# Optimization experiments

Measured on AMD Instinct MI355X. Metric: run time of the kernel, lower is better.

Reference implementation:

```python
import jax, jax.numpy as jnp
import numpy as np

B, T, D, DO = 8, 2048, 1024, 1024

def setup_inputs() -> dict:
    key = jax.random.key(0)
    ks = jax.random.split(key, 7)
    s = 1.0 / np.sqrt(D)
    return {
        "input_tensor": jax.random.normal(ks[0], (B, T, D), dtype=jnp.float32),
        "Wq": jax.random.uniform(ks[1], (D, D), jnp.float32, -s, s),
        "bq": jax.random.uniform(ks[2], (D,), jnp.float32, -s, s),
        "Wk": jax.random.uniform(ks[3], (D, D), jnp.float32, -s, s),
        "bk": jax.random.uniform(ks[4], (D,), jnp.float32, -s, s),
        "Wv": jax.random.uniform(ks[5], (D, DO), jnp.float32, -s, s),
        "bv": jax.random.uniform(ks[6], (DO,), jnp.float32, -s, s),
    }

def reference(input_tensor, Wq, bq, Wk, bk, Wv, bv):
    scale = jnp.sqrt(jnp.float32(input_tensor.shape[-1]))
    q = input_tensor @ Wq + bq            # [B,T,D]
    k = input_tensor @ Wk + bk            # [B,T,D]
    v = input_tensor @ Wv + bv            # [B,T,DO]
    scores = jnp.einsum('btd,bsd->bts', q, k) / scale  # [B,T,T]
    attn = jax.nn.softmax(scores, axis=-1)
    return jnp.einsum('bts,bso->bto', attn, v)         # [B,T,DO]
```

## Files before the change

kernel.cpp:

```cpp
#include <hip/hip_runtime.h>
#include <stdint.h>

typedef unsigned short u16;
typedef __attribute__((ext_vector_type(4))) float    floatx4;
typedef __attribute__((ext_vector_type(8))) __bf16   bf16x8;
typedef __attribute__((ext_vector_type(2))) unsigned int uintx2;
typedef __attribute__((ext_vector_type(4))) unsigned int uintx4;

__device__ inline u16 f2bf(float f) {
  unsigned int u = __builtin_bit_cast(unsigned int, f);
  u += 0x7fffu + ((u >> 16) & 1u);
  return (u16)(u >> 16);
}

#define GLD16(gsrc, ldst)                                                        \
  __builtin_amdgcn_global_load_lds(                                              \
      (__attribute__((address_space(1))) void*)(gsrc),                           \
      (__attribute__((address_space(3))) void*)(ldst), 16, 0, 0)

__global__ __launch_bounds__(256) void prep_kernel(const float* __restrict__ x,
                                                   const float* __restrict__ Wq,
                                                   const float* __restrict__ Wk,
                                                   const float* __restrict__ Wv,
                                                   u16* __restrict__ xb,
                                                   u16* __restrict__ WT) {
  const int z = blockIdx.z;
  const int tid = threadIdx.y * 32 + threadIdx.x;
  if (z >= 3) {
    long blk = (long)(z - 3) * 1024 + blockIdx.y * 32 + blockIdx.x;
    long i = (blk * 256 + tid) * 8;
    floatx4 a = *(const floatx4*)(x + i);
    floatx4 b = *(const floatx4*)(x + i + 4);
    uintx4 o;
    o[0] = (unsigned)f2bf(a[0]) | ((unsigned)f2bf(a[1]) << 16);
    o[1] = (unsigned)f2bf(a[2]) | ((unsigned)f2bf(a[3]) << 16);
    o[2] = (unsigned)f2bf(b[0]) | ((unsigned)f2bf(b[1]) << 16);
    o[3] = (unsigned)f2bf(b[2]) | ((unsigned)f2bf(b[3]) << 16);
    *(uintx4*)(xb + i) = o;
    return;
  }
  __shared__ float tile[32][33];
  const float* W = (z == 0) ? Wq : (z == 1) ? Wk : Wv;
  u16* dst = WT + (long)z * 1024 * 1024;
  int bx = blockIdx.x * 32, by = blockIdx.y * 32;
  int tx = threadIdx.x, ty = threadIdx.y;
  for (int i = 0; i < 32; i += 8)
    tile[ty + i][tx] = W[(long)(by + ty + i) * 1024 + bx + tx];
  __syncthreads();
  for (int i = 0; i < 32; i += 8)
    dst[(long)(bx + ty + i) * 1024 + by + tx] = f2bf(tile[tx][ty + i]);
}

#define BM 256
#define BN 256
#define BK 64

template <int MODE, int GN>
__global__ __launch_bounds__(512, 2)
void gemm_bt(const u16* __restrict__ Aall, const u16* __restrict__ Ball,
             void* __restrict__ Call, void* __restrict__ C2,
             const float* __restrict__ bias, const float* __restrict__ bias2,
             float* __restrict__ lsum,
             int M, int N, int K, long aStride, long bStride, long cStride) {
  __shared__ __align__(16) u16 As[2][BM * BK];
  __shared__ __align__(16) u16 Bs[2][BN * BK];

  const int z = blockIdx.z;
  const u16* A  = Aall + (long)z * aStride;
  const u16* Bt = Ball + (long)z * bStride;

  int m_idx, n_idx;
  if (GN > 0) {
    const int tiles_n = gridDim.x, tiles_m = gridDim.y;
    int bid = blockIdx.y * tiles_n + blockIdx.x;
    int per_group = GN * tiles_m;
    int g = bid / per_group;
    int rem = bid - g * per_group;
    n_idx = g * GN + rem % GN;
    m_idx = rem / GN;
  } else {
    m_idx = blockIdx.y; n_idx = blockIdx.x;
  }

  const int tid  = threadIdx.x;
  const int m0   = m_idx * BM;
  const int n0   = n_idx * BN;
  const int wave = tid >> 6;
  const int lane = tid & 63;
  const int wm   = (wave >> 2) * 128;
  const int wn   = (wave & 3) * 64;
  const int l15  = lane & 15;
  const int quad = lane >> 4;

  floatx4 acc[8][4];
  floatx4 zero = {0.f, 0.f, 0.f, 0.f};
#pragma unroll
  for (int i = 0; i < 8; ++i)
#pragma unroll
    for (int j = 0; j < 4; ++j) acc[i][j] = zero;

  int rows[4], cols[4];
#pragma unroll
  for (int i = 0; i < 4; ++i) {
    int ci = i * 512 + tid;
    int r = ci >> 3, sc = ci & 7;
    rows[i] = r; cols[i] = (sc ^ (r & 7)) * 8;
  }

  auto stage = [&](int kt, u16* as, u16* bs) {
#pragma unroll
    for (int i = 0; i < 4; ++i)
      GLD16(A + (long)(m0 + rows[i]) * K + kt + cols[i], as + (i * 512 + tid) * 8);
#pragma unroll
    for (int i = 0; i < 4; ++i)
      GLD16(Bt + (long)(n0 + rows[i]) * K + kt + cols[i], bs + (i * 512 + tid) * 8);
  };

  const int nt = K / BK;
  stage(0, As[0], Bs[0]);
  stage(BK, As[1], Bs[1]);

  for (int t = 0; t < nt; ++t) {
    const int cur = t & 1;
    const u16* Ab = As[cur];
    const u16* Bb = Bs[cur];
    if (t + 1 < nt) asm volatile("s_waitcnt vmcnt(8)" ::: "memory");
    else            asm volatile("s_waitcnt vmcnt(0)" ::: "memory");
    __builtin_amdgcn_s_barrier();
    __builtin_amdgcn_sched_barrier(0);

    bf16x8 af0[8], bf0[4], af1[8], bf1[4];
#pragma unroll
    for (int mi = 0; mi < 8; ++mi) {
      int r = wm + mi * 16 + l15;
      af0[mi] = *(const bf16x8*)(Ab + (r * 8 + (quad ^ (r & 7))) * 8);
    }
#pragma unroll
    for (int ni = 0; ni < 4; ++ni) {
      int r = wn + ni * 16 + l15;
      bf0[ni] = *(const bf16x8*)(Bb + (r * 8 + (quad ^ (r & 7))) * 8);
    }
    __builtin_amdgcn_s_setprio(1);
#pragma unroll
    for (int mi = 0; mi < 8; ++mi)
#pragma unroll
      for (int ni = 0; ni < 4; ++ni)
        acc[mi][ni] = __builtin_amdgcn_mfma_f32_16x16x32_bf16(
            bf0[ni], af0[mi], acc[mi][ni], 0, 0, 0);
    __builtin_amdgcn_s_setprio(0);
#pragma unroll
    for (int mi = 0; mi < 8; ++mi) {
      int r = wm + mi * 16 + l15;
      af1[mi] = *(const bf16x8*)(Ab + (r * 8 + ((4 + quad) ^ (r & 7))) * 8);
    }
#pragma unroll
    for (int ni = 0; ni < 4; ++ni) {
      int r = wn + ni * 16 + l15;
      bf1[ni] = *(const bf16x8*)(Bb + (r * 8 + ((4 + quad) ^ (r & 7))) * 8);
    }
    asm volatile("s_waitcnt lgkmcnt(0)" ::: "memory");
    __builtin_amdgcn_sched_barrier(0);
    __builtin_amdgcn_s_barrier();
    __builtin_amdgcn_sched_barrier(0);
    if (t + 2 < nt) stage((t + 2) * BK, As[cur], Bs[cur]);
    __builtin_amdgcn_s_setprio(1);
#pragma unroll
    for (int mi = 0; mi < 8; ++mi)
#pragma unroll
      for (int ni = 0; ni < 4; ++ni)
        acc[mi][ni] = __builtin_amdgcn_mfma_f32_16x16x32_bf16(
            bf1[ni], af1[mi], acc[mi][ni], 0, 0, 0);
    __builtin_amdgcn_s_setprio(0);
  }

#pragma unroll
  for (int mi = 0; mi < 8; ++mi) {
    const int row = m0 + wm + mi * 16 + l15;
    if (MODE == 2) {
      u16* C = (u16*)Call + (long)z * cStride;
      float rs = 0.f;
#pragma unroll
      for (int ni = 0; ni < 4; ++ni) {
        int colb = n0 + wn + ni * 16 + quad * 4;
        floatx4 v = acc[mi][ni];
        float e0 = __expf(v[0] * 0.03125f), e1 = __expf(v[1] * 0.03125f);
        float e2 = __expf(v[2] * 0.03125f), e3 = __expf(v[3] * 0.03125f);
        rs += (e0 + e1) + (e2 + e3);
        uintx2 o;
        o[0] = (unsigned)f2bf(e0) | ((unsigned)f2bf(e1) << 16);
        o[1] = (unsigned)f2bf(e2) | ((unsigned)f2bf(e3) << 16);
        *(uintx2*)(C + (long)row * N + colb) = o;
      }
      rs += __shfl_xor(rs, 16);
      rs += __shfl_xor(rs, 32);
      if (quad == 0) atomicAdd(lsum + (long)z * 2048 + row, rs);
    } else if (MODE == 3) {
      float* C = (float*)Call + (long)z * cStride;
      float inv = 1.0f / lsum[(long)z * 2048 + row];
#pragma unroll
      for (int ni = 0; ni < 4; ++ni) {
        int colb = n0 + wn + ni * 16 + quad * 4;
        floatx4 v = acc[mi][ni];
        floatx4 o = {v[0] * inv, v[1] * inv, v[2] * inv, v[3] * inv};
        *(floatx4*)(C + (long)row * N + colb) = o;
      }
    } else if (MODE == 0) {
#pragma unroll
      for (int ni = 0; ni < 4; ++ni) {
        int colb = n0 + wn + ni * 16 + quad * 4;
        u16* C = (colb < 1024) ? (u16*)Call : (u16*)C2;
        const float* bp = (colb < 1024) ? bias + colb : bias2 + (colb - 1024);
        floatx4 b = *(const floatx4*)bp;
        floatx4 v = acc[mi][ni];
        uintx2 o;
        o[0] = (unsigned)f2bf(v[0] + b[0]) | ((unsigned)f2bf(v[1] + b[1]) << 16);
        o[1] = (unsigned)f2bf(v[2] + b[2]) | ((unsigned)f2bf(v[3] + b[3]) << 16);
        *(uintx2*)(C + (long)row * 1024 + (colb & 1023)) = o;
      }
    } else {
      u16* C = (u16*)Call;
      float b = bias[row];
#pragma unroll
      for (int ni = 0; ni < 4; ++ni) {
        int colb = n0 + wn + ni * 16 + quad * 4;
        long base = ((long)(colb >> 11) * 1024) * 2048 + (colb & 2047);
        floatx4 v = acc[mi][ni];
        uintx2 o;
        o[0] = (unsigned)f2bf(v[0] + b) | ((unsigned)f2bf(v[1] + b) << 16);
        o[1] = (unsigned)f2bf(v[2] + b) | ((unsigned)f2bf(v[3] + b) << 16);
        *(uintx2*)(C + base + (long)row * 2048) = o;
      }
    }
  }
}

extern "C" void kernel_launch(void* const* d_in, const int* in_sizes, int n_in,
                              void* d_out, int out_size, void* d_ws, size_t ws_size,
                              hipStream_t stream) {
  const float* x  = (const float*)d_in[0];
  const float* Wq = (const float*)d_in[1];
  const float* bq = (const float*)d_in[2];
  const float* Wk = (const float*)d_in[3];
  const float* bk = (const float*)d_in[4];
  const float* Wv = (const float*)d_in[5];
  const float* bv = (const float*)d_in[6];
  float* out = (float*)d_out;

  const long BT = 16384;
  u16* xb = (u16*)d_ws;
  u16* WT = xb + BT * 1024;
  u16* qb = WT + 3L * 1024 * 1024;
  u16* kb = qb + BT * 1024;
  u16* vT = kb + BT * 1024;
  u16* S  = vT + BT * 1024;
  float* lsum = (float*)(S + 8L * 2048 * 2048);

  hipMemsetAsync(lsum, 0, 8 * 2048 * sizeof(float), stream);

  prep_kernel<<<dim3(32, 32, 11), dim3(32, 8), 0, stream>>>(x, Wq, Wk, Wv, xb, WT);

  gemm_bt<0, 8><<<dim3(8, 64, 1), 512, 0, stream>>>(
      xb, WT, qb, kb, bq, bk, nullptr, 16384, 2048, 1024, 0, 0, 0);
  gemm_bt<1, 8><<<dim3(64, 4, 1), 512, 0, stream>>>(
      WT + 2L * 1024 * 1024, xb, vT, nullptr, bv, nullptr, nullptr,
      1024, 16384, 1024, 0, 0, 0);
  gemm_bt<2, 8><<<dim3(8, 8, 8), 512, 0, stream>>>(
      qb, kb, S, nullptr, nullptr, nullptr, lsum,
      2048, 2048, 1024, 2048L * 1024, 2048L * 1024, 2048L * 2048);
  gemm_bt<3, 4><<<dim3(4, 8, 8), 512, 0, stream>>>(
      S, vT, out, nullptr, nullptr, nullptr, lsum,
      2048, 1024, 2048, 2048L * 2048, 1024L * 2048, 2048L * 1024);
}
```

Baseline: 384.4 us.

## Interleave global-to-LDS staging with four MFMA sub-phases per K tile

Restructures the GEMM main loop from two half-K MFMA phases with one bulk prefetch into four quarter phases. Each phase issues a slice of the next tile's A/B global_load_lds copies, with finer-grained vmcnt waits and barriers. The goal is to spread memory traffic across the MFMA work and cut register pressure from fragment arrays, so load latency hides better. In exchange it adds barriers per iteration and a fragile ordering of which buffer slices are overwritten when.

```diff
diff --git a/kernel.cpp b/kernel.cpp
--- a/kernel.cpp
+++ b/kernel.cpp
@@ -107,70 +107,130 @@
     rows[i] = r; cols[i] = (sc ^ (r & 7)) * 8;
   }
 
-  auto stage = [&](int kt, u16* as, u16* bs) {
-#pragma unroll
-    for (int i = 0; i < 4; ++i)
-      GLD16(A + (long)(m0 + rows[i]) * K + kt + cols[i], as + (i * 512 + tid) * 8);
-#pragma unroll
-    for (int i = 0; i < 4; ++i)
-      GLD16(Bt + (long)(n0 + rows[i]) * K + kt + cols[i], bs + (i * 512 + tid) * 8);
+  auto stageA = [&](int kt2, u16* dst, int b) {
+    GLD16(A + (long)(m0 + rows[b]) * K + kt2 + cols[b], dst + (b * 512 + tid) * 8);
   };
+  auto stageB = [&](int kt2, u16* dst, int b) {
+    GLD16(Bt + (long)(n0 + rows[b]) * K + kt2 + cols[b], dst + (b * 512 + tid) * 8);
+  };
 
   const int nt = K / BK;
-  stage(0, As[0], Bs[0]);
-  stage(BK, As[1], Bs[1]);
+
+  stageA(0, As[0], 0); stageA(0, As[0], 2);
+  stageB(0, Bs[0], 0); stageB(0, Bs[0], 1);
+  stageB(0, Bs[0], 2); stageB(0, Bs[0], 3);
+  stageA(0, As[0], 1); stageA(0, As[0], 3);
+  stageA(BK, As[1], 0); stageA(BK, As[1], 2);
+  asm volatile("s_waitcnt vmcnt(2)" ::: "memory");
+  __builtin_amdgcn_sched_barrier(0);
+  __builtin_amdgcn_s_barrier();
+  __builtin_amdgcn_sched_barrier(0);
 
   for (int t = 0; t < nt; ++t) {
     const int cur = t & 1;
     const u16* Ab = As[cur];
     const u16* Bb = Bs[cur];
-    if (t + 1 < nt) asm volatile("s_waitcnt vmcnt(8)" ::: "memory");
-    else            asm volatile("s_waitcnt vmcnt(0)" ::: "memory");
-    __builtin_amdgcn_s_barrier();
-    __builtin_amdgcn_sched_barrier(0);
-
-    bf16x8 af0[8], bf0[4], af1[8], bf1[4];
-#pragma unroll
-    for (int mi = 0; mi < 8; ++mi) {
+    u16* Ac = As[cur];
+    u16* An = As[cur ^ 1];
+    u16* Bn = Bs[cur ^ 1];
+    const int ktn = (t + 1) * BK;
+    const bool st1 = (t + 1 < nt);
+    const bool st2 = (t + 2 < nt);
+    bf16x8 afA[4], afB[4], bfr[4];
+
+#pragma unroll
+    for (int mi = 0; mi < 4; ++mi) {
       int r = wm + mi * 16 + l15;
-      af0[mi] = *(const bf16x8*)(Ab + (r * 8 + (quad ^ (r & 7))) * 8);
+      afA[mi] = *(const bf16x8*)(Ab + (r * 8 + (quad ^ (r & 7))) * 8);
     }
 #pragma unroll
     for (int ni = 0; ni < 4; ++ni) {
       int r = wn + ni * 16 + l15;
-      bf0[ni] = *(const bf16x8*)(Bb + (r * 8 + (quad ^ (r & 7))) * 8);
-    }
+      bfr[ni] = *(const bf16x8*)(Bb + (r * 8 + (quad ^ (r & 7))) * 8);
+    }
+    if (st1) { stageB(ktn, Bn, 0); stageB(ktn, Bn, 1); }
+    if (st1) asm volatile("s_waitcnt vmcnt(4)" ::: "memory");
+    else     asm volatile("s_waitcnt vmcnt(0)" ::: "memory");
+    asm volatile("s_waitcnt lgkmcnt(0)" ::: "memory");
+    __builtin_amdgcn_sched_barrier(0);
+    __builtin_amdgcn_s_barrier();
+    __builtin_amdgcn_sched_barrier(0);
     __builtin_amdgcn_s_setprio(1);
 #pragma unroll
-    for (int mi = 0; mi < 8; ++mi)
+    for (int mi = 0; mi < 4; ++mi)
 #pragma unroll
       for (int ni = 0; ni < 4; ++ni)
         acc[mi][ni] = __builtin_amdgcn_mfma_f32_16x16x32_bf16(
-            bf0[ni], af0[mi], acc[mi][ni], 0, 0, 0);
+            bfr[ni], afA[mi], acc[mi][ni], 0, 0, 0);
     __builtin_amdgcn_s_setprio(0);
-#pragma unroll
-    for (int mi = 0; mi < 8; ++mi) {
+    __builtin_amdgcn_sched_barrier(0);
+
+#pragma unroll
+    for (int mi = 0; mi < 4; ++mi) {
+      int r = wm + (4 + mi) * 16 + l15;
+      afB[mi] = *(const bf16x8*)(Ab + (r * 8 + (quad ^ (r & 7))) * 8);
+    }
+    if (st1) { stageB(ktn, Bn, 2); stageB(ktn, Bn, 3); }
+    asm volatile("s_waitcnt lgkmcnt(0)" ::: "memory");
+    __builtin_amdgcn_sched_barrier(0);
+    __builtin_amdgcn_s_barrier();
+    __builtin_amdgcn_sched_barrier(0);
+    __builtin_amdgcn_s_setprio(1);
+#pragma unroll
+    for (int mi = 0; mi < 4; ++mi)
+#pragma unroll
+      for (int ni = 0; ni < 4; ++ni)
+        acc[4 + mi][ni] = __builtin_amdgcn_mfma_f32_16x16x32_bf16(
+            bfr[ni], afB[mi], acc[4 + mi][ni], 0, 0, 0);
+    __builtin_amdgcn_s_setprio(0);
+    __builtin_amdgcn_sched_barrier(0);
+
+#pragma unroll
+    for (int mi = 0; mi < 4; ++mi) {
       int r = wm + mi * 16 + l15;
-      af1[mi] = *(const bf16x8*)(Ab + (r * 8 + ((4 + quad) ^ (r & 7))) * 8);
+      afA[mi] = *(const bf16x8*)(Ab + (r * 8 + ((4 + quad) ^ (r & 7))) * 8);
     }
 #pragma unroll
     for (int ni = 0; ni < 4; ++ni) {
       int r = wn + ni * 16 + l15;
-      bf1[ni] = *(const bf16x8*)(Bb + (r * 8 + ((4 + quad) ^ (r & 7))) * 8);
-    }
+      bfr[ni] = *(const bf16x8*)(Bb + (r * 8 + ((4 + quad) ^ (r & 7))) * 8);
+    }
+    if (st1) { stageA(ktn, An, 1); stageA(ktn, An, 3); }
     asm volatile("s_waitcnt lgkmcnt(0)" ::: "memory");
     __builtin_amdgcn_sched_barrier(0);
     __builtin_amdgcn_s_barrier();
     __builtin_amdgcn_sched_barrier(0);
-    if (t + 2 < nt) stage((t + 2) * BK, As[cur], Bs[cur]);
     __builtin_amdgcn_s_setprio(1);
 #pragma unroll
-    for (int mi = 0; mi < 8; ++mi)
+    for (int mi = 0; mi < 4; ++mi)
 #pragma unroll
       for (int ni = 0; ni < 4; ++ni)
         acc[mi][ni] = __builtin_amdgcn_mfma_f32_16x16x32_bf16(
-            bf1[ni], af1[mi], acc[mi][ni], 0, 0, 0);
+            bfr[ni], afA[mi], acc[mi][ni], 0, 0, 0);
     __builtin_amdgcn_s_setprio(0);
+    __builtin_amdgcn_sched_barrier(0);
+
+#pragma unroll
+    for (int mi = 0; mi < 4; ++mi) {
+      int r = wm + (4 + mi) * 16 + l15;
+      afB[mi] = *(const bf16x8*)(Ab + (r * 8 + ((4 + quad) ^ (r & 7))) * 8);
+    }
+    if (st2) { stageA(ktn + BK, Ac, 0); stageA(ktn + BK, Ac, 2); }
+    if (st2)      asm volatile("s_waitcnt vmcnt(4)" ::: "memory");
+    else if (st1) asm volatile("s_waitcnt vmcnt(2)" ::: "memory");
+    asm volatile("s_waitcnt lgkmcnt(0)" ::: "memory");
+    __builtin_amdgcn_sched_barrier(0);
+    __builtin_amdgcn_s_barrier();
+    __builtin_amdgcn_sched_barrier(0);
+    __builtin_amdgcn_s_setprio(1);
+#pragma unroll
+    for (int mi = 0; mi < 4; ++mi)
+#pragma unroll
+      for (int ni = 0; ni < 4; ++ni)
+        acc[4 + mi][ni] = __builtin_amdgcn_mfma_f32_16x16x32_bf16(
+            bfr[ni], afB[mi], acc[4 + mi][ni], 0, 0, 0);
+    __builtin_amdgcn_s_setprio(0);
+    __builtin_amdgcn_sched_barrier(0);
   }
 
 #pragma unroll
```

Measured after the change: 387.7 us. Within noise of the previous version (+0.8%).
